# Performance work log

Hardware: AMD Instinct MI355X
Metric: run time of the kernel (lower is better)

Reference implementation:

```python
import jax
import jax.numpy as jnp
import numpy as np

B, C, H, W = 32, 192, 28, 28
OUT, K, GROUPS = 384, 9, 4


def setup_inputs() -> dict:
    key = jax.random.key(0)
    k1, k2, k3 = jax.random.split(key, 3)
    x = jax.random.normal(k1, (B, C, H, W), dtype=jnp.float32)
    # 1x1 grouped conv (groups=4): weight [out_channels, in_channels*2 // groups]
    weight = jax.random.normal(k2, (OUT, 2 * C // GROUPS), dtype=jnp.float32) * 0.05
    bias = jax.random.normal(k3, (OUT,), dtype=jnp.float32) * 0.05
    return {"x": x, "weight": weight, "bias": bias}


def _knn_indices(xf, k):
    """xf: [B, C, N] node features. Returns nn_idx [B, N, k] (no grad)."""
    xf = jax.lax.stop_gradient(xf)
    # L2-normalize along channel dim (F.normalize p=2 dim=1, eps=1e-12)
    nrm = jnp.sqrt(jnp.sum(xf * xf, axis=1, keepdims=True))
    xn = xf / jnp.maximum(nrm, 1e-12)
    pts = jnp.transpose(xn, (0, 2, 1))  # [B, N, C]
    sq = jnp.sum(pts * pts, axis=-1)  # [B, N]
    # dist = ||x_i||^2 - 2 x_i.y_j + ||y_j||^2
    dist = sq[:, :, None] - 2.0 * jnp.einsum("bnc,bmc->bnm", pts, pts) + sq[:, None, :]
    _, nn_idx = jax.lax.top_k(-dist, k)  # smallest distances -> [B, N, k]
    return nn_idx


def reference(x, weight, bias):
    b, c, h, w = x.shape
    n = h * w
    xf = x.reshape(b, c, n)  # [B, C, N]

    nn_idx = _knn_indices(xf, K)  # [B, N, K]

    feat = jnp.transpose(xf, (0, 2, 1))  # [B, N, C]
    # gather neighbor features: x_j [B, C, N, K]
    x_j = jax.vmap(lambda f, i: f[i])(feat, nn_idx)  # [B, N, K, C]
    x_j = jnp.transpose(x_j, (0, 3, 1, 2))  # [B, C, N, K]
    x_i = xf[:, :, :, None]  # [B, C, N, 1] (center = identity gather)

    # EdgeConv features: cat([x_i, x_j - x_i]) -> [B, 2C, N, K]
    edge = jnp.concatenate(
        [jnp.broadcast_to(x_i, x_j.shape), x_j - x_i], axis=1
    )

    # 1x1 grouped conv (groups=4) + bias + exact GELU
    cin_g = 2 * c // GROUPS
    cout_g = OUT // GROUPS
    eg = edge.reshape(b, GROUPS, cin_g, n, K)
    wg = weight.reshape(GROUPS, cout_g, cin_g)
    y = jnp.einsum("bgcnk,goc->bgonk", eg, wg).reshape(b, OUT, n, K)
    y = y + bias[None, :, None, None]
    y = jax.nn.gelu(y, approximate=False)

    # max over neighbors
    y = jnp.max(y, axis=-1)  # [B, OUT, N]
    return y.reshape(b, OUT, h, w)
```

## Files before the change

kernel.cpp:

```cpp
#include <hip/hip_runtime.h>
#include <math.h>

#define BSZ 32
#define CCH 192
#define NPIX 784
#define NP 896
#define NGRP 56
#define NGU 49
#define OUTC 384
#define KNN 9

typedef short s8v __attribute__((ext_vector_type(8)));
typedef float f4v __attribute__((ext_vector_type(4)));

#define XFH_BYTES ((size_t)BSZ * NGRP * 6 * 64 * 8 * 2)
#define XFL_BYTES XFH_BYTES
#define PAIR_BYTES ((size_t)BSZ * NP * 8)
#define IDX_BYTES ((size_t)BSZ * NPIX * KNN * 4)
#define TBUF_BYTES ((size_t)BSZ * 192 * NPIX * 4)
#define WF_BYTES ((size_t)24 * 3 * 64 * 8 * 2)

__device__ __forceinline__ ushort bf16_rne(float f) {
    uint u = __float_as_uint(f);
    uint r = (u + 0x7fffu + ((u >> 16) & 1u)) >> 16;
    return (ushort)r;
}
__device__ __forceinline__ float bf16f(ushort h) { return __uint_as_float(((uint)h) << 16); }

__device__ __forceinline__ float gelu_fast(float u) {
    float x = u * 0.70710678118654752440f;
    float ax = fabsf(x);
    float t = __builtin_amdgcn_rcpf(fmaf(0.3275911f, ax, 1.0f));
    float p = t * fmaf(t, fmaf(t, fmaf(t, fmaf(t, 1.061405429f, -1.453152027f),
                                       1.421413741f), -0.284496736f), 0.254829592f);
    float e = __expf(-ax * ax);
    float erf_ax = fmaf(-p, e, 1.0f);
    float erfx = copysignf(erf_ax, x);
    return 0.5f * u * (1.0f + erfx);
}

__global__ __launch_bounds__(64) void k0_wfrag(const float* __restrict__ w,
                                               ushort* __restrict__ wfh,
                                               ushort* __restrict__ wfl) {
    int c2 = blockIdx.x;
    int l = threadIdx.x;
    int ob = c2 / 3, kc = c2 - ob * 3;
    int row = ob * 16 + (l & 15);
    int k0c = kc * 32 + (l >> 4) * 8;
    const float* wr = w + row * 96 + k0c;
    s8v hv, lv;
#pragma unroll
    for (int k = 0; k < 8; ++k) {
        float v = wr[k];
        ushort h = bf16_rne(v);
        hv[k] = (short)h;
        lv[k] = (short)bf16_rne(v - bf16f(h));
    }
    *(s8v*)(wfh + ((size_t)c2 * 64 + l) * 8) = hv;
    *(s8v*)(wfl + ((size_t)c2 * 64 + l) * 8) = lv;
}

__global__ __launch_bounds__(256) void k1_normalize(const float* __restrict__ x,
                                                    ushort* __restrict__ xfh,
                                                    ushort* __restrict__ xfl,
                                                    float2* __restrict__ pair) {
    __shared__ float xs[CCH][65];
    int b = blockIdx.y;
    int n0 = blockIdx.x * 64;
    int t = threadIdx.x;
    const float* xb = x + (size_t)b * CCH * NPIX;

    for (int i = t; i < CCH * 64; i += 256) {
        int c = i >> 6, j = i & 63, n = n0 + j;
        xs[c][j] = (n < NPIX) ? xb[c * NPIX + n] : 0.f;
    }
    __syncthreads();

    {
        int j = t >> 2, part = t & 3;
        float ss = 0.f;
        for (int k = 0; k < 48; ++k) { float v = xs[part * 48 + k][j]; ss = fmaf(v, v, ss); }
        ss += __shfl_xor(ss, 1);
        ss += __shfl_xor(ss, 2);
        float inv = 1.0f / fmaxf(sqrtf(ss), 1e-12f);
        float s2 = 0.f;
        for (int k = 0; k < 48; ++k) {
            float v = xs[part * 48 + k][j] * inv;
            s2 = fmaf(v, v, s2);
        }
        s2 += __shfl_xor(s2, 1);
        s2 += __shfl_xor(s2, 2);
        if (part == 0) {
            int n = n0 + j;
            pair[b * NP + n] = (n < NPIX) ? make_float2(s2, inv) : make_float2(1e30f, 0.f);
        }
    }

#pragma unroll
    for (int i = 0; i < 6; ++i) {
        int ch = t + i * 256;
        int g = ch / 384, rem = ch - g * 384;
        int kc = rem >> 6, l = rem & 63;
        int nl = g * 16 + (l & 15);
        int c0 = kc * 32 + (l >> 4) * 8;
        s8v hv, lv;
#pragma unroll
        for (int k = 0; k < 8; ++k) {
            float v = xs[c0 + k][nl];
            ushort h = bf16_rne(v);
            hv[k] = (short)h;
            lv[k] = (short)bf16_rne(v - bf16f(h));
        }
        size_t doff = (((size_t)(b * NGRP + (n0 >> 4) + g)) * 6 + kc) * 512 + (size_t)l * 8;
        *(s8v*)(xfh + doff) = hv;
        *(s8v*)(xfl + doff) = lv;
    }
}

__device__ __forceinline__ bool lt_pair(float v, int id, float dv, int di) {
    return (v < dv) || (v == dv && id < di);
}
__device__ __forceinline__ void ins9b(float (&d)[KNN], int (&ii)[KNN], float v, int id) {
    bool c[KNN];
#pragma unroll
    for (int p = 0; p < KNN; ++p) c[p] = v < d[p];
    float nd[KNN]; int ni[KNN];
    nd[0] = c[0] ? v : d[0];
    ni[0] = c[0] ? id : ii[0];
#pragma unroll
    for (int p = 1; p < KNN; ++p) {
        nd[p] = c[p - 1] ? d[p - 1] : (c[p] ? v : d[p]);
        ni[p] = c[p - 1] ? ii[p - 1] : (c[p] ? id : ii[p]);
    }
#pragma unroll
    for (int p = 0; p < KNN; ++p) { d[p] = nd[p]; ii[p] = ni[p]; }
}

__global__ __launch_bounds__(256) void k2_knn(const ushort* __restrict__ xfh,
                                              const ushort* __restrict__ xfl,
                                              const float* __restrict__ pair,
                                              int* __restrict__ nnidx) {
    __shared__ float dls[4][64][KNN];
    __shared__ int   ils[4][64][KNN];
    int wg = blockIdx.x;
    int b  = (wg & 7) * 4 + (wg >> 3) / 49;
    int qt = (wg >> 3) % 49;
    int t = threadIdx.x, w = t >> 6, l = t & 63;
    int lk = l >> 4;
    const ushort* fh = xfh + (size_t)b * NGRP * 3072;
    const ushort* fl = xfl + (size_t)b * NGRP * 3072;
    const float2* pb = (const float2*)(pair + (size_t)b * NP * 2);
    int l8 = l * 8;

    s8v qh[6], ql[6];
#pragma unroll
    for (int kc = 0; kc < 6; ++kc) {
        qh[kc] = *(const s8v*)(fh + (size_t)qt * 3072 + kc * 512 + l8);
        ql[kc] = *(const s8v*)(fl + (size_t)qt * 3072 + kc * 512 + l8);
    }
    float c2q = -2.f * pb[qt * 16 + (l & 15)].y;

    float d9[KNN]; int i9[KNN];
#pragma unroll
    for (int r = 0; r < KNN; ++r) { d9[r] = 3.4e38f; i9[r] = 0x7fffffff; }

    int g0 = (w == 0) ? 0 : w * 12 + 1;
    int g1 = g0 + ((w == 0) ? 13 : 12);
#pragma unroll 2
    for (int cg = g0; cg < g1; ++cg) {
        const ushort* ch = fh + (size_t)cg * 3072 + l8;
        const ushort* cl = fl + (size_t)cg * 3072 + l8;
        f4v aH  = {0.f, 0.f, 0.f, 0.f};
        f4v aX1 = {0.f, 0.f, 0.f, 0.f};
        f4v aX2 = {0.f, 0.f, 0.f, 0.f};
        f4v aX3 = {0.f, 0.f, 0.f, 0.f};
#pragma unroll
        for (int kc = 0; kc < 6; ++kc) {
            s8v vh = *(const s8v*)(ch + kc * 512);
            s8v vl = *(const s8v*)(cl + kc * 512);
            aH  = __builtin_amdgcn_mfma_f32_16x16x32_bf16(vh, qh[kc], aH,  0, 0, 0);
            aX1 = __builtin_amdgcn_mfma_f32_16x16x32_bf16(vl, qh[kc], aX1, 0, 0, 0);
            aX2 = __builtin_amdgcn_mfma_f32_16x16x32_bf16(vh, ql[kc], aX2, 0, 0, 0);
            aX3 = __builtin_amdgcn_mfma_f32_16x16x32_bf16(vl, ql[kc], aX3, 0, 0, 0);
        }
        float4 pA = *(const float4*)(pb + (size_t)(cg * 16 + lk * 4));
        float4 pB = *(const float4*)(pb + (size_t)(cg * 16 + lk * 4) + 2);
        float sqn_[4] = {pA.x, pA.z, pB.x, pB.z};
        float inv_[4] = {pA.y, pA.w, pB.y, pB.w};
#pragma unroll
        for (int r = 0; r < 4; ++r) {
            float v = fmaf(c2q * inv_[r], aH[r] + aX1[r] + aX2[r] + aX3[r], sqn_[r]);
            ins9b(d9, i9, v, cg * 16 + lk * 4 + r);
        }
    }

#pragma unroll
    for (int r = 0; r < KNN; ++r) { dls[w][l][r] = d9[r]; ils[w][l][r] = i9[r]; }
    __syncthreads();
    if (t < 16) {
        int q = qt * 16 + t;
        int pk[16];
#pragma unroll
        for (int m = 0; m < 16; ++m) pk[m] = 0;
        int* op = nnidx + ((size_t)b * NPIX + q) * KNN;
        for (int r = 0; r < KNN; ++r) {
            float best = 3.4e38f; int bi = 0x7fffffff; int bk = 0;
#pragma unroll
            for (int m = 0; m < 16; ++m) {
                int ww = m >> 2, kk = m & 3;
                int idx = pk[m] < KNN ? pk[m] : KNN - 1;
                float v = dls[ww][kk * 16 + t][idx];
                int ii = ils[ww][kk * 16 + t][idx];
                if (pk[m] < KNN && lt_pair(v, ii, best, bi)) { best = v; bi = ii; bk = m; }
            }
            op[r] = bi;
#pragma unroll
            for (int m = 0; m < 16; ++m) pk[m] += (m == bk) ? 1 : 0;
        }
    }
}

__global__ __launch_bounds__(256, 2) void k3_proj(const ushort* __restrict__ xfh,
                                                  const ushort* __restrict__ xfl,
                                                  const ushort* __restrict__ wfh,
                                                  const ushort* __restrict__ wfl,
                                                  const float* __restrict__ bias,
                                                  float* __restrict__ out,
                                                  float* __restrict__ tbuf) {
    int wg = blockIdx.x;
    int b  = (wg & 7) * 4 + (wg >> 3) / 49;
    int ng = (wg >> 3) % 49;
    int t = threadIdx.x, g = t >> 6, l = t & 63;
    int h = l >> 4, m16 = l & 15;
    int kb = (g & 1) * 3;
    int l8 = l * 8;

    const ushort* fh = xfh + (((size_t)(b * NGRP + ng)) * 6 + kb) * 512 + l8;
    const ushort* fl = xfl + (((size_t)(b * NGRP + ng)) * 6 + kb) * 512 + l8;
    s8v xh[3], xl[3];
#pragma unroll
    for (int kk = 0; kk < 3; ++kk) {
        xh[kk] = *(const s8v*)(fh + kk * 512);
        xl[kk] = *(const s8v*)(fl + kk * 512);
    }

    for (int ogg = 0; ogg < 6; ++ogg) {
        int ob = g * 6 + ogg;
        const ushort* ph = wfh + ((size_t)ob * 3) * 512 + l8;
        const ushort* pl = wfl + ((size_t)ob * 3) * 512 + l8;
        f4v acc = {0.f, 0.f, 0.f, 0.f};
#pragma unroll
        for (int kk = 0; kk < 3; ++kk) {
            s8v wh = *(const s8v*)(ph + kk * 512);
            s8v wl = *(const s8v*)(pl + kk * 512);
            acc = __builtin_amdgcn_mfma_f32_16x16x32_bf16(xh[kk], wh, acc, 0, 0, 0);
            acc = __builtin_amdgcn_mfma_f32_16x16x32_bf16(xh[kk], wl, acc, 0, 0, 0);
            acc = __builtin_amdgcn_mfma_f32_16x16x32_bf16(xl[kk], wh, acc, 0, 0, 0);
        }
        int row = g * 96 + ogg * 16 + m16;
        if (g < 2) {
            float bv = bias[row];
#pragma unroll
            for (int r = 0; r < 4; ++r) {
                int n = ng * 16 + h * 4 + r;
                out[((size_t)b * OUTC + row) * NPIX + n] = gelu_fast(acc[r] + bv);
            }
        } else {
            int r2 = (g - 2) * 96 + ogg * 16 + m16;
#pragma unroll
            for (int r = 0; r < 4; ++r) {
                int n = ng * 16 + h * 4 + r;
                tbuf[((size_t)b * 192 + r2) * NPIX + n] = acc[r];
            }
        }
    }
}

__global__ __launch_bounds__(256) void k4_gather(const float* __restrict__ tbuf,
                                                 const int* __restrict__ nnidx,
                                                 const float* __restrict__ bias,
                                                 float* __restrict__ out) {
    __shared__ float trow[NPIX];
    __shared__ int nn[NPIX * KNN];
    int wg = blockIdx.x;
    int b   = (wg & 7) * 4 + (wg >> 3) / 24;
    int oct = (wg >> 3) % 24;
    int t = threadIdx.x;
    const int4* nb4 = (const int4*)(nnidx + (size_t)b * NPIX * KNN);
    for (int i = t; i < NPIX * KNN / 4; i += 256) ((int4*)nn)[i] = nb4[i];

    for (int oo = 0; oo < 8; ++oo) {
        int og2 = oct * 8 + oo;
        const float4* tr4 = (const float4*)(tbuf + ((size_t)b * 192 + og2) * NPIX);
        for (int i = t; i < NPIX / 4; i += 256) ((float4*)trow)[i] = tr4[i];
        __syncthreads();
        float bv = bias[192 + og2];
        float* orow = out + ((size_t)b * OUTC + 192 + og2) * NPIX;
        for (int n = t; n < NPIX; n += 256) {
            float ti = trow[n];
            const int* ip = nn + n * KNN;
            float umin = 3.4e38f, umax = -3.4e38f;
#pragma unroll
            for (int k = 0; k < KNN; ++k) {
                int j = ip[k];
                float u = trow[j] - ti + bv;
                umin = fminf(umin, u);
                umax = fmaxf(umax, u);
            }
            orow[n] = fmaxf(gelu_fast(umin), gelu_fast(umax));
        }
        __syncthreads();
    }
}

extern "C" void kernel_launch(void* const* d_in, const int* in_sizes, int n_in,
                              void* d_out, int out_size, void* d_ws, size_t ws_size,
                              hipStream_t stream) {
    const float* x    = (const float*)d_in[0];
    const float* w    = (const float*)d_in[1];
    const float* bias = (const float*)d_in[2];
    float* out = (float*)d_out;
    char* ws = (char*)d_ws;

    ushort* xfh   = (ushort*)(ws);
    ushort* xfl   = (ushort*)(ws + XFH_BYTES);
    float2* pair  = (float2*)(ws + XFH_BYTES + XFL_BYTES);
    int*    nnidx = (int*)   (ws + XFH_BYTES + XFL_BYTES + PAIR_BYTES);
    float*  tbuf  = (float*) (ws + XFH_BYTES + XFL_BYTES + PAIR_BYTES + IDX_BYTES);
    ushort* wfh   = (ushort*)(ws + XFH_BYTES + XFL_BYTES + PAIR_BYTES + IDX_BYTES + TBUF_BYTES);
    ushort* wfl   = (ushort*)(ws + XFH_BYTES + XFL_BYTES + PAIR_BYTES + IDX_BYTES + TBUF_BYTES + WF_BYTES);

    k0_wfrag<<<dim3(72), 64, 0, stream>>>(w, wfh, wfl);
    k1_normalize<<<dim3(13, BSZ), 256, 0, stream>>>(x, xfh, xfl, pair);
    k2_knn<<<dim3(1568), 256, 0, stream>>>(xfh, xfl, (const float*)pair, nnidx);
    k3_proj<<<dim3(1568), 256, 0, stream>>>(xfh, xfl, wfh, wfl, bias, out, tbuf);
    k4_gather<<<dim3(768), 256, 0, stream>>>(tbuf, nnidx, bias, out);
}
```

Before: 142.7 us.

## Process two query tiles per KNN block, staging queries in LDS to reuse candidates

Each KNN workgroup now handles two 16-query tiles instead of one, so every candidate fragment loaded from global memory feeds twice as many MFMAs. The query fragments move from registers to shared memory so that two sets of top-9 lists can be held. This halves candidate traffic and the grid size, at the cost of more registers, extra LDS reads per MFMA, and one duplicated tile when the tile count is odd (qt1 is clamped to 48, so that tile is recomputed and rewritten). Launch bounds are set to 3 waves per SIMD.

```diff
diff --git a/kernel.cpp b/kernel.cpp
--- a/kernel.cpp
+++ b/kernel.cpp
@@ -136,15 +136,18 @@
     for (int p = 0; p < KNN; ++p) { d[p] = nd[p]; ii[p] = ni[p]; }
 }
 
-__global__ __launch_bounds__(256) void k2_knn(const ushort* __restrict__ xfh,
-                                              const ushort* __restrict__ xfl,
-                                              const float* __restrict__ pair,
-                                              int* __restrict__ nnidx) {
+__global__ __launch_bounds__(256, 3) void k2_knn(const ushort* __restrict__ xfh,
+                                                 const ushort* __restrict__ xfl,
+                                                 const float* __restrict__ pair,
+                                                 int* __restrict__ nnidx) {
+    __shared__ ushort qlds[2][6144];
     __shared__ float dls[4][64][KNN];
     __shared__ int   ils[4][64][KNN];
     int wg = blockIdx.x;
-    int b  = (wg & 7) * 4 + (wg >> 3) / 49;
-    int qt = (wg >> 3) % 49;
+    int b  = (wg & 7) * 4 + (wg >> 3) / 25;
+    int qp = (wg >> 3) % 25;
+    int qt0 = qp * 2;
+    int qt1 = (qp * 2 + 1 > 48) ? 48 : qp * 2 + 1;
     int t = threadIdx.x, w = t >> 6, l = t & 63;
     int lk = l >> 4;
     const ushort* fh = xfh + (size_t)b * NGRP * 3072;
@@ -152,53 +155,97 @@
     const float2* pb = (const float2*)(pair + (size_t)b * NP * 2);
     int l8 = l * 8;
 
-    s8v qh[6], ql[6];
-#pragma unroll
-    for (int kc = 0; kc < 6; ++kc) {
-        qh[kc] = *(const s8v*)(fh + (size_t)qt * 3072 + kc * 512 + l8);
-        ql[kc] = *(const s8v*)(fl + (size_t)qt * 3072 + kc * 512 + l8);
-    }
-    float c2q = -2.f * pb[qt * 16 + (l & 15)].y;
-
-    float d9[KNN]; int i9[KNN];
-#pragma unroll
-    for (int r = 0; r < KNN; ++r) { d9[r] = 3.4e38f; i9[r] = 0x7fffffff; }
-
-    int g0 = (w == 0) ? 0 : w * 12 + 1;
-    int g1 = g0 + ((w == 0) ? 13 : 12);
-#pragma unroll 2
+    for (int i = t; i < 1536; i += 256) {
+        int qg = i / 768, rem = i - qg * 768;
+        int half = rem / 384, off = (rem - half * 384) * 8;
+        int qtg = qg ? qt1 : qt0;
+        s8v v = *(const s8v*)((half ? fl : fh) + (size_t)qtg * 3072 + off);
+        *(s8v*)(&qlds[qg][half * 3072 + off]) = v;
+    }
+    float c2qA = -2.f * pb[qt0 * 16 + (l & 15)].y;
+    float c2qB = -2.f * pb[qt1 * 16 + (l & 15)].y;
+    __syncthreads();
+
+    float d9A[KNN], d9B[KNN]; int i9A[KNN], i9B[KNN];
+#pragma unroll
+    for (int r = 0; r < KNN; ++r) {
+        d9A[r] = 3.4e38f; i9A[r] = 0x7fffffff;
+        d9B[r] = 3.4e38f; i9B[r] = 0x7fffffff;
+    }
+
+    const ushort* qpA = &qlds[0][0] + l8;
+    const ushort* qpB = &qlds[1][0] + l8;
+
+    int g0 = (w == 0) ? 0 : 13 + (w - 1) * 12;
+    int g1 = (w == 0) ? 13 : g0 + 12;
     for (int cg = g0; cg < g1; ++cg) {
         const ushort* ch = fh + (size_t)cg * 3072 + l8;
         const ushort* cl = fl + (size_t)cg * 3072 + l8;
-        f4v aH  = {0.f, 0.f, 0.f, 0.f};
-        f4v aX1 = {0.f, 0.f, 0.f, 0.f};
-        f4v aX2 = {0.f, 0.f, 0.f, 0.f};
-        f4v aX3 = {0.f, 0.f, 0.f, 0.f};
+        f4v aH0  = {0.f, 0.f, 0.f, 0.f}, aX10 = {0.f, 0.f, 0.f, 0.f};
+        f4v aX20 = {0.f, 0.f, 0.f, 0.f}, aX30 = {0.f, 0.f, 0.f, 0.f};
+        f4v aH1  = {0.f, 0.f, 0.f, 0.f}, aX11 = {0.f, 0.f, 0.f, 0.f};
+        f4v aX21 = {0.f, 0.f, 0.f, 0.f}, aX31 = {0.f, 0.f, 0.f, 0.f};
 #pragma unroll
         for (int kc = 0; kc < 6; ++kc) {
             s8v vh = *(const s8v*)(ch + kc * 512);
             s8v vl = *(const s8v*)(cl + kc * 512);
-            aH  = __builtin_amdgcn_mfma_f32_16x16x32_bf16(vh, qh[kc], aH,  0, 0, 0);
-            aX1 = __builtin_amdgcn_mfma_f32_16x16x32_bf16(vl, qh[kc], aX1, 0, 0, 0);
-            aX2 = __builtin_amdgcn_mfma_f32_16x16x32_bf16(vh, ql[kc], aX2, 0, 0, 0);
-            aX3 = __builtin_amdgcn_mfma_f32_16x16x32_bf16(vl, ql[kc], aX3, 0, 0, 0);
-        }
-        float4 pA = *(const float4*)(pb + (size_t)(cg * 16 + lk * 4));
-        float4 pB = *(const float4*)(pb + (size_t)(cg * 16 + lk * 4) + 2);
-        float sqn_[4] = {pA.x, pA.z, pB.x, pB.z};
-        float inv_[4] = {pA.y, pA.w, pB.y, pB.w};
+            s8v qhA = *(const s8v*)(qpA + kc * 512);
+            s8v qlA = *(const s8v*)(qpA + 3072 + kc * 512);
+            s8v qhB = *(const s8v*)(qpB + kc * 512);
+            s8v qlB = *(const s8v*)(qpB + 3072 + kc * 512);
+            aH0  = __builtin_amdgcn_mfma_f32_16x16x32_bf16(vh, qhA, aH0,  0, 0, 0);
+            aX10 = __builtin_amdgcn_mfma_f32_16x16x32_bf16(vl, qhA, aX10, 0, 0, 0);
+            aX20 = __builtin_amdgcn_mfma_f32_16x16x32_bf16(vh, qlA, aX20, 0, 0, 0);
+            aX30 = __builtin_amdgcn_mfma_f32_16x16x32_bf16(vl, qlA, aX30, 0, 0, 0);
+            aH1  = __builtin_amdgcn_mfma_f32_16x16x32_bf16(vh, qhB, aH1,  0, 0, 0);
+            aX11 = __builtin_amdgcn_mfma_f32_16x16x32_bf16(vl, qhB, aX11, 0, 0, 0);
+            aX21 = __builtin_amdgcn_mfma_f32_16x16x32_bf16(vh, qlB, aX21, 0, 0, 0);
+            aX31 = __builtin_amdgcn_mfma_f32_16x16x32_bf16(vl, qlB, aX31, 0, 0, 0);
+        }
+        float4 pA4 = *(const float4*)(pb + (size_t)(cg * 16 + lk * 4));
+        float4 pB4 = *(const float4*)(pb + (size_t)(cg * 16 + lk * 4) + 2);
+        float sqn_[4] = {pA4.x, pA4.z, pB4.x, pB4.z};
+        float inv_[4] = {pA4.y, pA4.w, pB4.y, pB4.w};
 #pragma unroll
         for (int r = 0; r < 4; ++r) {
-            float v = fmaf(c2q * inv_[r], aH[r] + aX1[r] + aX2[r] + aX3[r], sqn_[r]);
-            ins9b(d9, i9, v, cg * 16 + lk * 4 + r);
-        }
-    }
-
-#pragma unroll
-    for (int r = 0; r < KNN; ++r) { dls[w][l][r] = d9[r]; ils[w][l][r] = i9[r]; }
+            int id = cg * 16 + lk * 4 + r;
+            float vA = fmaf(c2qA * inv_[r], aH0[r] + aX10[r] + aX20[r] + aX30[r], sqn_[r]);
+            ins9b(d9A, i9A, vA, id);
+            float vB = fmaf(c2qB * inv_[r], aH1[r] + aX11[r] + aX21[r] + aX31[r], sqn_[r]);
+            ins9b(d9B, i9B, vB, id);
+        }
+    }
+
+#pragma unroll
+    for (int r = 0; r < KNN; ++r) { dls[w][l][r] = d9A[r]; ils[w][l][r] = i9A[r]; }
     __syncthreads();
     if (t < 16) {
-        int q = qt * 16 + t;
+        int q = qt0 * 16 + t;
+        int pk[16];
+#pragma unroll
+        for (int m = 0; m < 16; ++m) pk[m] = 0;
+        int* op = nnidx + ((size_t)b * NPIX + q) * KNN;
+        for (int r = 0; r < KNN; ++r) {
+            float best = 3.4e38f; int bi = 0x7fffffff; int bk = 0;
+#pragma unroll
+            for (int m = 0; m < 16; ++m) {
+                int ww = m >> 2, kk = m & 3;
+                int idx = pk[m] < KNN ? pk[m] : KNN - 1;
+                float v = dls[ww][kk * 16 + t][idx];
+                int ii = ils[ww][kk * 16 + t][idx];
+                if (pk[m] < KNN && lt_pair(v, ii, best, bi)) { best = v; bi = ii; bk = m; }
+            }
+            op[r] = bi;
+#pragma unroll
+            for (int m = 0; m < 16; ++m) pk[m] += (m == bk) ? 1 : 0;
+        }
+    }
+    __syncthreads();
+#pragma unroll
+    for (int r = 0; r < KNN; ++r) { dls[w][l][r] = d9B[r]; ils[w][l][r] = i9B[r]; }
+    __syncthreads();
+    if (t < 16) {
+        int q = qt1 * 16 + t;
         int pk[16];
 #pragma unroll
         for (int m = 0; m < 16; ++m) pk[m] = 0;
@@ -332,7 +379,7 @@
 
     k0_wfrag<<<dim3(72), 64, 0, stream>>>(w, wfh, wfl);
     k1_normalize<<<dim3(13, BSZ), 256, 0, stream>>>(x, xfh, xfl, pair);
-    k2_knn<<<dim3(1568), 256, 0, stream>>>(xfh, xfl, (const float*)pair, nnidx);
+    k2_knn<<<dim3(800), 256, 0, stream>>>(xfh, xfl, (const float*)pair, nnidx);
     k3_proj<<<dim3(1568), 256, 0, stream>>>(xfh, xfl, wfh, wfl, bias, out, tbuf);
     k4_gather<<<dim3(768), 256, 0, stream>>>(tbuf, nnidx, bias, out);
 }
```

New measurement: 247.7 us. 73.6% more time.
